# Kernel tuning notes

Hardware: AMD Instinct MI355X
Metric: run time of the kernel (lower is better)

## Reference

```python
import jax, jax.numpy as jnp
import numpy as np

B, K, N, D, E, EE, H, P = 512, 64, 1024, 128, 100000, 1024, 256, 12

def setup_inputs() -> dict:
    key = jax.random.key(0)
    ks = jax.random.split(key, 6)
    return {
        'ts_emb': jax.random.normal(ks[0], (B, D, N), jnp.float32),
        'event_table': jax.random.normal(ks[1], (E, EE), jnp.float32),
        'W_t': jax.random.normal(ks[2], (H, EE), jnp.float32) * 0.02,
        'b_t': jnp.zeros((H,), jnp.float32),
        'W_mm': jax.random.normal(ks[3], (P, H + D), jnp.float32) * 0.02,
        'b_mm': jnp.zeros((P,), jnp.float32),
        'W_ts': jax.random.normal(ks[4], (P, D), jnp.float32) * 0.02,
        'b_ts': jnp.zeros((P,), jnp.float32),
        'event_idx': jax.random.randint(ks[5], (B, K), 0, E, jnp.int64) if jax.config.read('jax_enable_x64') else jax.random.randint(ks[5], (B, K), 0, E, jnp.int32),
        'event_mask': jnp.ones((B, K), bool),
    }

def reference(ts_emb, event_table, W_t, b_t, W_mm, b_mm, W_ts, b_ts, event_idx, event_mask):
    h = W_t.shape[0]  # hidden_event_emb_dim
    # ragged event gather: [B, K, EE]
    ev = event_table[event_idx]
    # Linear(EE -> H): [B, K, H]
    ev_h = jnp.einsum('bke,he->bkh', ev, W_t) + b_t
    # masked max over events (event_fuse_type='max'): [B, H]
    neg = jnp.asarray(-jnp.inf, ev_h.dtype)
    ev_emb = jnp.max(jnp.where(event_mask[:, :, None], ev_h, neg), axis=1)
    # mm_forecaster = Conv1d(H+D -> P, k=1) on cat([event_emb repeat N, ts_emb]);
    # split the channel-wise linear so the broadcast part is never materialized.
    mm_ev = ev_emb @ W_mm[:, :h].T                       # [B, P]
    mm_ts = jnp.einsum('pd,bdn->bpn', W_mm[:, h:], ts_emb)  # [B, P, N]
    mm_pred = mm_ev[:, :, None] + mm_ts + b_mm[None, :, None]
    # ts_forecaster = Conv1d(D -> P, k=1)
    ts_pred = jnp.einsum('pd,bdn->bpn', W_ts, ts_emb) + b_ts[None, :, None]
    return (ts_pred + mm_pred) * 0.5
```

## Files before the change

kernel.cpp:

```cpp
#include <hip/hip_runtime.h>
#include <hip/hip_bf16.h>
#include <math.h>

#define B_   512
#define KEV  64
#define NN   1024
#define DD   128
#define EE_  1024
#define HH   256
#define PP   12
#define BK   128
#define NSTEP (EE_ / BK)

typedef __bf16 bf16x8 __attribute__((ext_vector_type(8)));
typedef float  f32x4  __attribute__((ext_vector_type(4)));
typedef unsigned short ushort8_t __attribute__((ext_vector_type(8)));

static __device__ __forceinline__ unsigned short f2bf(float f) {
    unsigned int u = __builtin_bit_cast(unsigned int, f);
    u = (u + 0x7FFFu + ((u >> 16) & 1u)) >> 16;
    return (unsigned short)u;
}

__global__ __launch_bounds__(256) void prep_kernel(
    const float* __restrict__ Wt,
    const float* __restrict__ Wmm,
    const float* __restrict__ Wts,
    const unsigned int* __restrict__ idxW,
    const unsigned int* __restrict__ mskW,
    unsigned short* __restrict__ WtBf,
    float* __restrict__ Wc,
    int* __restrict__ flags)
{
    if (blockIdx.x < 256) {
        int i4 = (blockIdx.x * 256 + threadIdx.x) * 4;
        const float4 v = *reinterpret_cast<const float4*>(Wt + i4);
        ushort4 o = make_ushort4(f2bf(v.x), f2bf(v.y), f2bf(v.z), f2bf(v.w));
        *reinterpret_cast<ushort4*>(WtBf + i4) = o;
        return;
    }
    __shared__ int any_nz;
    if (threadIdx.x == 0) any_nz = 0;
    __syncthreads();
    int local = 0;
    for (int k = threadIdx.x; k < (B_ * KEV) / 2; k += 256)
        local |= (idxW[2 * k + 1] != 0u);
    if (local) atomicOr(&any_nz, 1);
    for (int k = threadIdx.x; k < PP * DD; k += 256) {
        int p = k >> 7, d = k & 127;
        Wc[k] = Wmm[p * (HH + DD) + HH + d] + Wts[p * DD + d];
    }
    __syncthreads();
    if (threadIdx.x == 0) {
        flags[0] = any_nz ? 0 : 1;
        unsigned int w0 = mskW[0], w1 = mskW[1];
        flags[1] = (w0 == 0x01010101u) ? 0 : ((w1 == 0u) ? 2 : 1);
    }
}

__global__ __launch_bounds__(256, 2) void mega_kernel(
    const float* __restrict__ ts,
    const float* __restrict__ Wc,
    const float* __restrict__ table,
    const void* __restrict__ idxRaw,
    const void* __restrict__ maskRaw,
    const int* __restrict__ flags,
    const unsigned short* __restrict__ WtBf,
    const float* __restrict__ bt,
    const float* __restrict__ Wmm,
    const float* __restrict__ bmm,
    const float* __restrict__ bts,
    float* __restrict__ cOut,
    float* __restrict__ out)
{
    const int t = threadIdx.x;

    __shared__ __align__(16) unsigned short sA[2][64 * BK];
    __shared__ int           sIdx[KEV];
    __shared__ unsigned char sMask[KEV];
    __shared__ float         sEv[HH];

    if (blockIdx.x < B_) {
        const int b = blockIdx.x;
        const float* tsb = ts + (size_t)b * DD * NN + (t << 2);

        f32x4 tacc[PP];
        #pragma unroll
        for (int p = 0; p < PP; ++p) tacc[p] = (f32x4){0.f, 0.f, 0.f, 0.f};

        #pragma unroll 2
        for (int d0 = 0; d0 < DD; d0 += 8) {
            f32x4 v[8];
            #pragma unroll
            for (int j = 0; j < 8; ++j)
                v[j] = __builtin_nontemporal_load(
                    reinterpret_cast<const f32x4*>(tsb + (size_t)(d0 + j) * NN));
            #pragma unroll
            for (int j = 0; j < 8; ++j) {
                #pragma unroll
                for (int p = 0; p < PP; ++p)
                    tacc[p] += Wc[p * DD + d0 + j] * v[j];
            }
        }

        float* ob = out + (size_t)b * PP * NN + (t << 2);
        #pragma unroll
        for (int p = 0; p < PP; ++p) {
            const f32x4 r = tacc[p] * 0.5f;
            __builtin_nontemporal_store(r,
                reinterpret_cast<f32x4*>(ob + (size_t)p * NN));
        }
        return;
    }

    const int b = blockIdx.x - B_;

    if (t < KEV) {
        const int i = b * KEV + t;
        int id;
        if (flags[0]) id = (int)((const long long*)idxRaw)[i];
        else          id = ((const int*)idxRaw)[i];
        sIdx[t] = id;
        const int mm = flags[1];
        bool mk;
        if      (mm == 0) mk = ((const unsigned char*)maskRaw)[i] != 0;
        else if (mm == 1) mk = ((const int*)maskRaw)[i] != 0;
        else              mk = ((const long long*)maskRaw)[i] != 0;
        sMask[t] = mk ? 1 : 0;
    }
    __syncthreads();

    const int srow  = t >> 2;
    const int seoff = (t & 3) * 32;
    const float* rowp = table + (size_t)sIdx[srow] * EE_ + seoff;

    auto loadstep = [&](int s, float4 (&r)[8]) {
        const float4* p = reinterpret_cast<const float4*>(rowp + s * BK);
        #pragma unroll
        for (int j = 0; j < 8; ++j) r[j] = p[j];
    };
    auto writebuf = [&](int bufi, const float4 (&r)[8]) {
        unsigned short* base = &sA[bufi][srow * BK];
        const int swz = ((srow & 7) << 3) ^ ((srow & 8) << 1);
        #pragma unroll
        for (int j = 0; j < 4; ++j) {
            const float4 a = r[2 * j], c = r[2 * j + 1];
            ushort8_t o;
            o[0]=f2bf(a.x); o[1]=f2bf(a.y); o[2]=f2bf(a.z); o[3]=f2bf(a.w);
            o[4]=f2bf(c.x); o[5]=f2bf(c.y); o[6]=f2bf(c.z); o[7]=f2bf(c.w);
            *reinterpret_cast<ushort8_t*>(base + ((seoff + j * 8) ^ swz)) = o;
        }
    };

    const int w    = t >> 6;
    const int lane = t & 63;
    const int lm   = lane & 15;
    const int lg   = lane >> 4;

    f32x4 acc[4][4];
    #pragma unroll
    for (int mi = 0; mi < 4; ++mi)
        #pragma unroll
        for (int ni = 0; ni < 4; ++ni)
            acc[mi][ni] = (f32x4){0.f, 0.f, 0.f, 0.f};

    const unsigned short* wtB = WtBf + (size_t)(w * 64 + lm) * EE_ + lg * 8;

    auto mfma_step = [&](int cur, int s) {
        #pragma unroll
        for (int ks = 0; ks < 4; ++ks) {
            bf16x8 af[4];
            #pragma unroll
            for (int mi = 0; mi < 4; ++mi) {
                const int row = mi * 16 + lm;
                const int e   = ks * 32 + lg * 8;
                const int es  = e ^ ((row & 7) << 3) ^ ((row & 8) << 1);
                af[mi] = *reinterpret_cast<const bf16x8*>(&sA[cur][row * BK + es]);
            }
            #pragma unroll
            for (int ni = 0; ni < 4; ++ni) {
                const unsigned short* bp = wtB + (size_t)ni * 16 * EE_ + s * BK + ks * 32;
                bf16x8 bfr = *reinterpret_cast<const bf16x8*>(bp);
                #pragma unroll
                for (int mi = 0; mi < 4; ++mi)
                    acc[mi][ni] = __builtin_amdgcn_mfma_f32_16x16x32_bf16(
                        af[mi], bfr, acc[mi][ni], 0, 0, 0);
            }
        }
    };

    float4 rA[8], rB[8];
    loadstep(0, rA);
    writebuf(0, rA);
    loadstep(1, rA);
    __syncthreads();

    #pragma unroll
    for (int ss = 0; ss < NSTEP / 2; ++ss) {
        {
            const int s = 2 * ss;
            if (s + 2 < NSTEP) loadstep(s + 2, rB);
            mfma_step(s & 1, s);
            writebuf((s + 1) & 1, rA);
            __syncthreads();
        }
        {
            const int s = 2 * ss + 1;
            if (s + 2 < NSTEP) loadstep(s + 2, rA);
            mfma_step(s & 1, s);
            if (s + 1 < NSTEP) writebuf((s + 1) & 1, rB);
            __syncthreads();
        }
    }

    #pragma unroll
    for (int ni = 0; ni < 4; ++ni) {
        float mx = -INFINITY;
        #pragma unroll
        for (int mi = 0; mi < 4; ++mi) {
            #pragma unroll
            for (int r = 0; r < 4; ++r) {
                const int ev = mi * 16 + lg * 4 + r;
                const float v = sMask[ev] ? acc[mi][ni][r] : -INFINITY;
                mx = fmaxf(mx, v);
            }
        }
        mx = fmaxf(mx, __shfl_xor(mx, 16));
        mx = fmaxf(mx, __shfl_xor(mx, 32));
        if (lg == 0) {
            const int h = w * 64 + ni * 16 + lm;
            sEv[h] = mx + bt[h];
        }
    }
    __syncthreads();

    if (w == 0) {
        #pragma unroll 1
        for (int p = 0; p < PP; ++p) {
            const float* wr = Wmm + p * (HH + DD);
            float sum = sEv[lane]       * wr[lane]
                      + sEv[lane + 64]  * wr[lane + 64]
                      + sEv[lane + 128] * wr[lane + 128]
                      + sEv[lane + 192] * wr[lane + 192];
            #pragma unroll
            for (int off = 32; off >= 1; off >>= 1) sum += __shfl_xor(sum, off);
            if (lane == 0) cOut[b * PP + p] = sum + bmm[p] + bts[p];
        }
    }
}

__global__ __launch_bounds__(256) void addc_kernel(
    const float* __restrict__ cIn,
    float* __restrict__ out)
{
    const int b = blockIdx.x;
    const int t = threadIdx.x;

    __shared__ float sC[PP];
    if (t < PP) sC[t] = 0.5f * cIn[b * PP + t];
    __syncthreads();

    float* ob = out + (size_t)b * PP * NN + (t << 2);
    #pragma unroll
    for (int p = 0; p < PP; ++p) {
        const float c = sC[p];
        f32x4 v = *reinterpret_cast<const f32x4*>(ob + (size_t)p * NN);
        v += (f32x4){c, c, c, c};
        __builtin_nontemporal_store(v, reinterpret_cast<f32x4*>(ob + (size_t)p * NN));
    }
}

extern "C" void kernel_launch(void* const* d_in, const int* in_sizes, int n_in,
                              void* d_out, int out_size, void* d_ws, size_t ws_size,
                              hipStream_t stream)
{
    const float* ts    = (const float*)d_in[0];
    const float* table = (const float*)d_in[1];
    const float* Wt    = (const float*)d_in[2];
    const float* bt    = (const float*)d_in[3];
    const float* Wmm   = (const float*)d_in[4];
    const float* bmm   = (const float*)d_in[5];
    const float* Wts   = (const float*)d_in[6];
    const float* bts   = (const float*)d_in[7];
    const void*  idx   = (const void*)d_in[8];
    const void*  msk   = (const void*)d_in[9];
    float* out = (float*)d_out;

    unsigned short* WtBf = (unsigned short*)d_ws;
    float* Wc  = (float*)((char*)d_ws + (512u << 10));
    float* cB  = (float*)((char*)d_ws + (512u << 10) + 8192);
    int*   flg = (int*)((char*)d_ws + (512u << 10) + 8192 + B_ * PP * 4);

    prep_kernel<<<257, 256, 0, stream>>>(Wt, Wmm, Wts,
                                         (const unsigned int*)idx,
                                         (const unsigned int*)msk,
                                         WtBf, Wc, flg);
    mega_kernel<<<2 * B_, 256, 0, stream>>>(ts, Wc, table, idx, msk, flg,
                                            WtBf, bt, Wmm, bmm, bts, cB, out);
    addc_kernel<<<B_, 256, 0, stream>>>(cB, out);
}
```

Baseline: 122.4 us.

## Interleave ts and event blocks, widen gather K-tile, restructure pipeline

Block indices now alternate in groups of 256 between the ts-projection work and the event gather/GEMM work, so the two kinds of work share the GPU at the same time instead of running as separate halves. The event path doubles its K tile to 256, which doubles LDS per buffer to 64 KB total and may limit occupancy. It also replaces the two-register-set double buffer with a single-register prefetch loop that is not unrolled. The ts path processes 16 channels per iteration and uses plain stores instead of nontemporal stores, which raises register pressure.

```diff
diff --git a/kernel.cpp b/kernel.cpp
--- a/kernel.cpp
+++ b/kernel.cpp
@@ -9,8 +9,8 @@
 #define EE_  1024
 #define HH   256
 #define PP   12
-#define BK   128
-#define NSTEP (EE_ / BK)
+#define BKE  256
+#define NSE  (EE_ / BKE)
 
 typedef __bf16 bf16x8 __attribute__((ext_vector_type(8)));
 typedef float  f32x4  __attribute__((ext_vector_type(4)));
@@ -73,30 +73,33 @@
     float* __restrict__ cOut,
     float* __restrict__ out)
 {
-    const int t = threadIdx.x;
-
-    __shared__ __align__(16) unsigned short sA[2][64 * BK];
+    const int t     = threadIdx.x;
+    const int g     = blockIdx.x;
+    const int phase = g >> 8;
+    const int sub   = g & 255;
+    const int b     = ((phase >> 1) << 8) | sub;
+
+    __shared__ __align__(16) unsigned short sA[2][64 * BKE];
     __shared__ int           sIdx[KEV];
     __shared__ unsigned char sMask[KEV];
     __shared__ float         sEv[HH];
 
-    if (blockIdx.x < B_) {
-        const int b = blockIdx.x;
+    if ((phase & 1) == 0) {
         const float* tsb = ts + (size_t)b * DD * NN + (t << 2);
 
         f32x4 tacc[PP];
         #pragma unroll
         for (int p = 0; p < PP; ++p) tacc[p] = (f32x4){0.f, 0.f, 0.f, 0.f};
 
-        #pragma unroll 2
-        for (int d0 = 0; d0 < DD; d0 += 8) {
-            f32x4 v[8];
-            #pragma unroll
-            for (int j = 0; j < 8; ++j)
+        #pragma unroll 1
+        for (int d0 = 0; d0 < DD; d0 += 16) {
+            f32x4 v[16];
+            #pragma unroll
+            for (int j = 0; j < 16; ++j)
                 v[j] = __builtin_nontemporal_load(
                     reinterpret_cast<const f32x4*>(tsb + (size_t)(d0 + j) * NN));
             #pragma unroll
-            for (int j = 0; j < 8; ++j) {
+            for (int j = 0; j < 16; ++j) {
                 #pragma unroll
                 for (int p = 0; p < PP; ++p)
                     tacc[p] += Wc[p * DD + d0 + j] * v[j];
@@ -107,13 +110,10 @@
         #pragma unroll
         for (int p = 0; p < PP; ++p) {
             const f32x4 r = tacc[p] * 0.5f;
-            __builtin_nontemporal_store(r,
-                reinterpret_cast<f32x4*>(ob + (size_t)p * NN));
+            *reinterpret_cast<f32x4*>(ob + (size_t)p * NN) = r;
         }
         return;
     }
-
-    const int b = blockIdx.x - B_;
 
     if (t < KEV) {
         const int i = b * KEV + t;
@@ -131,19 +131,19 @@
     __syncthreads();
 
     const int srow  = t >> 2;
-    const int seoff = (t & 3) * 32;
+    const int seoff = (t & 3) * 64;
     const float* rowp = table + (size_t)sIdx[srow] * EE_ + seoff;
 
-    auto loadstep = [&](int s, float4 (&r)[8]) {
-        const float4* p = reinterpret_cast<const float4*>(rowp + s * BK);
-        #pragma unroll
-        for (int j = 0; j < 8; ++j) r[j] = p[j];
+    auto loadstep = [&](int s, float4 (&r)[16]) {
+        const float4* p = reinterpret_cast<const float4*>(rowp + s * BKE);
+        #pragma unroll
+        for (int j = 0; j < 16; ++j) r[j] = p[j];
     };
-    auto writebuf = [&](int bufi, const float4 (&r)[8]) {
-        unsigned short* base = &sA[bufi][srow * BK];
+    auto writebuf = [&](int bufi, const float4 (&r)[16]) {
+        unsigned short* base = &sA[bufi][srow * BKE];
         const int swz = ((srow & 7) << 3) ^ ((srow & 8) << 1);
         #pragma unroll
-        for (int j = 0; j < 4; ++j) {
+        for (int j = 0; j < 8; ++j) {
             const float4 a = r[2 * j], c = r[2 * j + 1];
             ushort8_t o;
             o[0]=f2bf(a.x); o[1]=f2bf(a.y); o[2]=f2bf(a.z); o[3]=f2bf(a.w);
@@ -168,18 +168,18 @@
 
     auto mfma_step = [&](int cur, int s) {
         #pragma unroll
-        for (int ks = 0; ks < 4; ++ks) {
+        for (int ks = 0; ks < 8; ++ks) {
             bf16x8 af[4];
             #pragma unroll
             for (int mi = 0; mi < 4; ++mi) {
                 const int row = mi * 16 + lm;
                 const int e   = ks * 32 + lg * 8;
                 const int es  = e ^ ((row & 7) << 3) ^ ((row & 8) << 1);
-                af[mi] = *reinterpret_cast<const bf16x8*>(&sA[cur][row * BK + es]);
+                af[mi] = *reinterpret_cast<const bf16x8*>(&sA[cur][row * BKE + es]);
             }
             #pragma unroll
             for (int ni = 0; ni < 4; ++ni) {
-                const unsigned short* bp = wtB + (size_t)ni * 16 * EE_ + s * BK + ks * 32;
+                const unsigned short* bp = wtB + (size_t)ni * 16 * EE_ + s * BKE + ks * 32;
                 bf16x8 bfr = *reinterpret_cast<const bf16x8*>(bp);
                 #pragma unroll
                 for (int mi = 0; mi < 4; ++mi)
@@ -189,28 +189,17 @@
         }
     };
 
-    float4 rA[8], rB[8];
+    float4 rA[16];
     loadstep(0, rA);
     writebuf(0, rA);
-    loadstep(1, rA);
-    __syncthreads();
-
-    #pragma unroll
-    for (int ss = 0; ss < NSTEP / 2; ++ss) {
-        {
-            const int s = 2 * ss;
-            if (s + 2 < NSTEP) loadstep(s + 2, rB);
-            mfma_step(s & 1, s);
-            writebuf((s + 1) & 1, rA);
-            __syncthreads();
-        }
-        {
-            const int s = 2 * ss + 1;
-            if (s + 2 < NSTEP) loadstep(s + 2, rA);
-            mfma_step(s & 1, s);
-            if (s + 1 < NSTEP) writebuf((s + 1) & 1, rB);
-            __syncthreads();
-        }
+    __syncthreads();
+
+    #pragma unroll 1
+    for (int s = 0; s < NSE; ++s) {
+        if (s + 1 < NSE) loadstep(s + 1, rA);
+        mfma_step(s & 1, s);
+        if (s + 1 < NSE) writebuf((s + 1) & 1, rA);
+        __syncthreads();
     }
 
     #pragma unroll
```

Result: no change. 120.4 us (-1.6%).

## Split event and ts work into separate kernels, fuse bias add into ts kernel

Applied to the files above, without the earlier changes.

The combined kernel that ran the ts projection and the event branch in separate block ranges is split into an event kernel and a ts kernel. The ts kernel now runs after the event kernel and adds the per-batch event bias directly, so the output is no longer read back and rewritten by a separate add pass. The ts projection is spread over four blocks per batch with the D reduction split across waves and combined through shared memory, which adds barriers. The trade-off is that the ts stream no longer overlaps with the gather-heavy event work.

```diff
diff --git a/kernel.cpp b/kernel.cpp
--- a/kernel.cpp
+++ b/kernel.cpp
@@ -58,9 +58,7 @@
     }
 }
 
-__global__ __launch_bounds__(256, 2) void mega_kernel(
-    const float* __restrict__ ts,
-    const float* __restrict__ Wc,
+__global__ __launch_bounds__(256, 2) void event_kernel(
     const float* __restrict__ table,
     const void* __restrict__ idxRaw,
     const void* __restrict__ maskRaw,
@@ -70,50 +68,15 @@
     const float* __restrict__ Wmm,
     const float* __restrict__ bmm,
     const float* __restrict__ bts,
-    float* __restrict__ cOut,
-    float* __restrict__ out)
+    float* __restrict__ cOut)
 {
+    const int b = blockIdx.x;
     const int t = threadIdx.x;
 
     __shared__ __align__(16) unsigned short sA[2][64 * BK];
     __shared__ int           sIdx[KEV];
     __shared__ unsigned char sMask[KEV];
     __shared__ float         sEv[HH];
-
-    if (blockIdx.x < B_) {
-        const int b = blockIdx.x;
-        const float* tsb = ts + (size_t)b * DD * NN + (t << 2);
-
-        f32x4 tacc[PP];
-        #pragma unroll
-        for (int p = 0; p < PP; ++p) tacc[p] = (f32x4){0.f, 0.f, 0.f, 0.f};
-
-        #pragma unroll 2
-        for (int d0 = 0; d0 < DD; d0 += 8) {
-            f32x4 v[8];
-            #pragma unroll
-            for (int j = 0; j < 8; ++j)
-                v[j] = __builtin_nontemporal_load(
-                    reinterpret_cast<const f32x4*>(tsb + (size_t)(d0 + j) * NN));
-            #pragma unroll
-            for (int j = 0; j < 8; ++j) {
-                #pragma unroll
-                for (int p = 0; p < PP; ++p)
-                    tacc[p] += Wc[p * DD + d0 + j] * v[j];
-            }
-        }
-
-        float* ob = out + (size_t)b * PP * NN + (t << 2);
-        #pragma unroll
-        for (int p = 0; p < PP; ++p) {
-            const f32x4 r = tacc[p] * 0.5f;
-            __builtin_nontemporal_store(r,
-                reinterpret_cast<f32x4*>(ob + (size_t)p * NN));
-        }
-        return;
-    }
-
-    const int b = blockIdx.x - B_;
 
     if (t < KEV) {
         const int i = b * KEV + t;
@@ -249,24 +212,69 @@
     }
 }
 
-__global__ __launch_bounds__(256) void addc_kernel(
+__global__ __launch_bounds__(256) void ts_kernel(
+    const float* __restrict__ ts,
+    const float* __restrict__ Wc,
     const float* __restrict__ cIn,
     float* __restrict__ out)
 {
-    const int b = blockIdx.x;
-    const int t = threadIdx.x;
-
+    const int t   = threadIdx.x;
+    const int b   = blockIdx.x >> 2;
+    const int cid = blockIdx.x & 3;
+    const int w   = t >> 6;
+    const int l   = t & 63;
+
+    __shared__ f32x4 sRed[PP * 64];
     __shared__ float sC[PP];
-    if (t < PP) sC[t] = 0.5f * cIn[b * PP + t];
-    __syncthreads();
-
-    float* ob = out + (size_t)b * PP * NN + (t << 2);
+
+    if (t < PP) sC[t] = cIn[b * PP + t];
+
+    const float* tsb = ts + (size_t)b * DD * NN + (size_t)(w * 32) * NN
+                          + cid * 256 + (l << 2);
+
+    f32x4 tacc[PP];
     #pragma unroll
-    for (int p = 0; p < PP; ++p) {
-        const float c = sC[p];
-        f32x4 v = *reinterpret_cast<const f32x4*>(ob + (size_t)p * NN);
-        v += (f32x4){c, c, c, c};
-        __builtin_nontemporal_store(v, reinterpret_cast<f32x4*>(ob + (size_t)p * NN));
+    for (int p = 0; p < PP; ++p) tacc[p] = (f32x4){0.f, 0.f, 0.f, 0.f};
+
+    #pragma unroll 1
+    for (int d0 = 0; d0 < 32; d0 += 8) {
+        f32x4 v[8];
+        #pragma unroll
+        for (int j = 0; j < 8; ++j)
+            v[j] = *reinterpret_cast<const f32x4*>(tsb + (size_t)(d0 + j) * NN);
+        #pragma unroll
+        for (int j = 0; j < 8; ++j) {
+            const int d = w * 32 + d0 + j;
+            #pragma unroll
+            for (int p = 0; p < PP; ++p)
+                tacc[p] += Wc[p * DD + d] * v[j];
+        }
+    }
+
+    if (w == 0) {
+        #pragma unroll
+        for (int p = 0; p < PP; ++p) sRed[p * 64 + l] = tacc[p];
+    }
+    __syncthreads();
+    if (w == 1) {
+        #pragma unroll
+        for (int p = 0; p < PP; ++p) sRed[p * 64 + l] += tacc[p];
+    }
+    __syncthreads();
+    if (w == 2) {
+        #pragma unroll
+        for (int p = 0; p < PP; ++p) sRed[p * 64 + l] += tacc[p];
+    }
+    __syncthreads();
+    if (w == 3) {
+        float* ob = out + (size_t)b * PP * NN + cid * 256 + (l << 2);
+        #pragma unroll
+        for (int p = 0; p < PP; ++p) {
+            const float c = sC[p];
+            const f32x4 r = (sRed[p * 64 + l] + tacc[p] + (f32x4){c, c, c, c}) * 0.5f;
+            __builtin_nontemporal_store(r,
+                reinterpret_cast<f32x4*>(ob + (size_t)p * NN));
+        }
     }
 }
 
@@ -295,7 +303,7 @@
                                          (const unsigned int*)idx,
                                          (const unsigned int*)msk,
                                          WtBf, Wc, flg);
-    mega_kernel<<<2 * B_, 256, 0, stream>>>(ts, Wc, table, idx, msk, flg,
-                                            WtBf, bt, Wmm, bmm, bts, cB, out);
-    addc_kernel<<<B_, 256, 0, stream>>>(cB, out);
-}
+    event_kernel<<<B_, 256, 0, stream>>>(table, idx, msk, flg, WtBf, bt,
+                                         Wmm, bmm, bts, cB);
+    ts_kernel<<<4 * B_, 256, 0, stream>>>(ts, Wc, cB, out);
+}
```

New measurement: 158.9 us. 29.8% more time.
